# Performance work log

Measured on AMD Instinct MI355X. Metric: run time of the kernel, lower is better.

Reference implementation:

```python
import jax, jax.numpy as jnp
import numpy as np

B, S, E, H = 4, 2048, 1024, 16
D = E // H  # head dim = 64
NEG = -1e9


def setup_inputs() -> dict:
    key = jax.random.key(0)
    ks = jax.random.split(key, 6)
    scale = 1.0 / np.sqrt(E)
    return {
        "x": jax.random.normal(ks[0], (B, S, E), dtype=jnp.float32),
        "in_proj_weight": jax.random.normal(ks[1], (3 * E, E), dtype=jnp.float32) * scale,
        "in_proj_bias": jax.random.normal(ks[2], (3 * E,), dtype=jnp.float32) * 0.02,
        "out_proj_weight": jax.random.normal(ks[3], (E, E), dtype=jnp.float32) * scale,
        "out_proj_bias": jax.random.normal(ks[4], (E,), dtype=jnp.float32) * 0.02,
        "mask": jax.random.randint(ks[5], (B, S), 0, 2, dtype=jnp.int32),
    }


def reference(x, in_proj_weight, in_proj_bias, out_proj_weight, out_proj_bias, mask):
    # Equivalent of F.multi_head_attention_forward(h,h,h,...) with batch-first x.
    # qkv projection: [B,S,3E]
    qkv = jnp.einsum("bse,fe->bsf", x, in_proj_weight) + in_proj_bias
    q, k, v = jnp.split(qkv, 3, axis=-1)
    # split heads -> [B,S,H,D]
    q = q.reshape(B, S, H, D) * (1.0 / np.sqrt(D))
    k = k.reshape(B, S, H, D)
    v = v.reshape(B, S, H, D)
    # scores [B,H,Sq,Sk]
    scores = jnp.einsum("bqhd,bkhd->bhqk", q, k)
    # key_padding_mask = (mask == 0): True positions are excluded
    pad = (mask == 0)[:, None, None, :]  # [B,1,1,Sk]
    scores = jnp.where(pad, NEG, scores)
    attn = jax.nn.softmax(scores, axis=-1)
    # attention output -> [B,S,E]
    ctx = jnp.einsum("bhqk,bkhd->bqhd", attn, v).reshape(B, S, E)
    h_ = jnp.einsum("bse,fe->bsf", ctx, out_proj_weight) + out_proj_bias
    # residual; dropout is identity in eval mode
    return x + h_
```

## Files before the change

### kernel.cpp

```cpp
#include <hip/hip_runtime.h>
#include <stdint.h>
#include <math.h>

#define B_ 4
#define S_ 2048
#define E_ 1024
#define H_ 16
#define D_ 64
#define M_ (B_*S_)

typedef __attribute__((ext_vector_type(8))) short bf16x8;
typedef __attribute__((ext_vector_type(4))) float f32x4;

__device__ __forceinline__ unsigned short f2bf(float f) {
  union { float f; uint32_t u; } v; v.f = f;
  uint32_t u = v.u;
  return (unsigned short)((u + 0x7FFFu + ((u >> 16) & 1u)) >> 16);
}

__device__ __forceinline__ void gload16(const void* g, void* l) {
  __builtin_amdgcn_global_load_lds(
      (__attribute__((address_space(1))) void*)g,
      (__attribute__((address_space(3))) void*)l, 16, 0, 0);
}

__device__ __forceinline__ uint32_t cvtpk(float lo, float hi) {
  uint32_t r;
  asm("v_cvt_pk_bf16_f32 %0, %1, %2" : "=v"(r) : "v"(lo), "v"(hi));
  return r;
}

#define N1 ((M_*E_)/4)
#define N2 ((3*E_*E_)/4)
#define N3 ((E_*E_)/4)
#define NM ((B_*S_)/4)
__global__ __launch_bounds__(256) void cvt_all(const float* __restrict__ x,
                                               const float* __restrict__ w1,
                                               const float* __restrict__ w2,
                                               const int* __restrict__ mask,
                                               unsigned short* __restrict__ dst,
                                               float* __restrict__ maskf) {
  int i = blockIdx.x * 256 + threadIdx.x;
  if (i < N1 + N2 + N3) {
    const float* src;
    int j;
    if (i < N1) { src = x; j = i; }
    else if (i < N1 + N2) { src = w1; j = i - N1; }
    else { src = w2; j = i - N1 - N2; }
    float4 v = reinterpret_cast<const float4*>(src)[j];
    ushort4 o;
    o.x = f2bf(v.x); o.y = f2bf(v.y); o.z = f2bf(v.z); o.w = f2bf(v.w);
    reinterpret_cast<ushort4*>(dst)[i] = o;
  } else if (i < N1 + N2 + N3 + NM) {
    int j = i - (N1 + N2 + N3);
    int4 m = reinterpret_cast<const int4*>(mask)[j];
    float4 o;
    o.x = m.x ? 0.0f : -2.0e9f;
    o.y = m.y ? 0.0f : -2.0e9f;
    o.z = m.z ? 0.0f : -2.0e9f;
    o.w = m.w ? 0.0f : -2.0e9f;
    reinterpret_cast<float4*>(maskf)[j] = o;
  }
}

__global__ __launch_bounds__(256) void gemm_qkv128(
    const unsigned short* __restrict__ A,
    const unsigned short* __restrict__ W,
    const float* __restrict__ bias,
    unsigned short* __restrict__ Qg,
    unsigned short* __restrict__ Kg,
    unsigned short* __restrict__ Vtg)
{
  __shared__ __align__(16) unsigned short SMEM[17408];
  unsigned short* As = SMEM;
  unsigned short* Bs = SMEM + 8192;
  const int tid = threadIdx.x;
  const int lane = tid & 63;
  const int wave = tid >> 6;
  const int wm = (wave >> 1) * 64, wn = (wave & 1) * 64;
  const int l15 = lane & 15, lg = lane >> 4;

  const int orig = blockIdx.y * 24 + blockIdx.x;
  const int xcd = orig & 7;
  const int idx = orig >> 3;
  const int tn = (xcd * 3 + (idx % 3)) * 128;
  const int tm = (idx / 3) * 128;

  f32x4 zero4 = {0.f, 0.f, 0.f, 0.f};
  f32x4 acc[4][4];
  #pragma unroll
  for (int mi = 0; mi < 4; ++mi)
    #pragma unroll
    for (int ni = 0; ni < 4; ++ni) acc[mi][ni] = zero4;

  const int r0 = tid >> 3;
  const int cg = ((tid & 7) ^ (r0 & 7)) * 8;
  const unsigned short* Abase = A + (size_t)(tm + r0) * E_ + cg;
  const unsigned short* Bbase = W + (size_t)(tn + r0) * E_ + cg;
  unsigned short* lA = As + tid * 8;
  unsigned short* lB = Bs + tid * 8;

  int aoff[4], boff[4];
  #pragma unroll
  for (int i = 0; i < 4; ++i) {
    aoff[i] = (wm + i*16 + l15)*64 + ((lg ^ (l15 & 7)) * 8);
    boff[i] = (wn + i*16 + l15)*64 + ((lg ^ (l15 & 7)) * 8);
  }
  const int x4a = ((lg ^ 4 ^ (l15 & 7)) * 8) - ((lg ^ (l15 & 7)) * 8);

  for (int k0 = 0; k0 < E_; k0 += 64) {
    #pragma unroll
    for (int j = 0; j < 4; ++j)
      gload16(Abase + k0 + j*32*E_, lA + j*2048);
    #pragma unroll
    for (int j = 0; j < 4; ++j)
      gload16(Bbase + k0 + j*32*E_, lB + j*2048);
    __syncthreads();
    #pragma unroll
    for (int kc = 0; kc < 2; ++kc) {
      bf16x8 af[4], bfv[4];
      #pragma unroll
      for (int mi = 0; mi < 4; ++mi)
        af[mi] = *(const bf16x8*)&As[aoff[mi] + kc*x4a];
      #pragma unroll
      for (int ni = 0; ni < 4; ++ni)
        bfv[ni] = *(const bf16x8*)&Bs[boff[ni] + kc*x4a];
      #pragma unroll
      for (int mi = 0; mi < 4; ++mi)
        #pragma unroll
        for (int ni = 0; ni < 4; ++ni)
          acc[mi][ni] = __builtin_amdgcn_mfma_f32_16x16x32_bf16(af[mi], bfv[ni], acc[mi][ni], 0, 0, 0);
    }
    __syncthreads();
  }

  const int sec = tn >> 10;
  if (sec < 2) {
    #pragma unroll
    for (int ni = 0; ni < 4; ++ni) {
      const int col = tn + wn + ni*16 + l15;
      const float bcol = bias[col];
      const int f2 = col & 1023;
      const int h = f2 >> 6, d = f2 & 63;
      #pragma unroll
      for (int mi = 0; mi < 4; ++mi) {
        #pragma unroll
        for (int r = 0; r < 4; ++r) {
          const int row = tm + wm + mi*16 + lg*4 + r;
          const int b = row >> 11, s = row & (S_-1);
          const size_t bh = (size_t)(b * H_ + h);
          float val = acc[mi][ni][r] + bcol;
          if (sec == 0) {
            Qg[(bh*S_ + s)*D_ + d] = f2bf(val * 0.18033688f);
          } else {
            const int ch = (d >> 3) ^ (s & 7);
            Kg[(bh*S_ + s)*D_ + ch*8 + (d & 7)] = f2bf(val);
          }
        }
      }
    }
  } else {
    __syncthreads();
    unsigned short* T = SMEM;
    #pragma unroll
    for (int ni = 0; ni < 4; ++ni) {
      const int f = wn + ni*16 + l15;
      const float bcol = bias[tn + f];
      #pragma unroll
      for (int mi = 0; mi < 4; ++mi) {
        const int s0 = wm + mi*16 + lg*4;
        uint2 p;
        p.x = cvtpk(acc[mi][ni][0] + bcol, acc[mi][ni][1] + bcol);
        p.y = cvtpk(acc[mi][ni][2] + bcol, acc[mi][ni][3] + bcol);
        *reinterpret_cast<uint2*>(&T[f*136 + s0]) = p;
      }
    }
    __syncthreads();
    const int f = tid >> 1, sch = tid & 1;
    const int d = f & 63, hl = f >> 6;
    const int h = ((tn & 1023) >> 6) + hl;
    const int b = tm >> 11;
    const size_t bh = (size_t)(b * H_ + h);
    const int sbase = (tm & (S_-1)) + sch*64;
    unsigned short* vout = Vtg + (bh*D_ + d)*S_ + sbase;
    const unsigned short* tin = &T[f*136 + sch*64];
    #pragma unroll
    for (int j = 0; j < 8; ++j) {
      uint4 v = *reinterpret_cast<const uint4*>(&tin[j*8]);
      *reinterpret_cast<uint4*>(&vout[(j ^ (d & 7))*8]) = v;
    }
  }
}

__global__ __launch_bounds__(512, 4) void attn_fwd(
    const unsigned short* __restrict__ Qg,
    const unsigned short* __restrict__ Kg,
    const unsigned short* __restrict__ Vtg,
    const float* __restrict__ maskf,
    unsigned short* __restrict__ ctx)
{
  __shared__ __align__(16) unsigned char SMEM[36864];
  unsigned short* KsP = (unsigned short*)SMEM;
  unsigned short* VsP = (unsigned short*)(SMEM + 16384);
  const int tid = threadIdx.x, lane = tid & 63, wave = tid >> 6;
  const int l15 = lane & 15, lg = lane >> 4;

  const int lin = blockIdx.x;
  const int bh = (lin & 7) * 8 + (lin >> 6);
  const int qi = (lin >> 3) & 7;
  const int b = bh >> 4, h = bh & 15;
  const int q0 = qi * 256 + wave * 32;

  const unsigned short* Qb = Qg + (size_t)bh * S_ * D_;
  const unsigned short* Kb = Kg + (size_t)bh * S_ * D_;
  const unsigned short* Vb = Vtg + (size_t)bh * D_ * S_;
  const float* mrow = maskf + b * S_;

  bf16x8 qf[2][2];
  #pragma unroll
  for (int mi = 0; mi < 2; ++mi)
    #pragma unroll
    for (int kc = 0; kc < 2; ++kc)
      qf[mi][kc] = *(const bf16x8*)&Qb[(size_t)(q0 + mi*16 + l15)*D_ + kc*32 + lg*8];

  f32x4 zero4 = {0.f, 0.f, 0.f, 0.f};
  f32x4 accO[2][4];
  f32x4 accL[2] = {zero4, zero4};
  #pragma unroll
  for (int mi = 0; mi < 2; ++mi)
    #pragma unroll
    for (int df = 0; df < 4; ++df) accO[mi][df] = zero4;

  union { uint32_t u[4]; bf16x8 v; } ou;
  ou.u[0] = ou.u[1] = ou.u[2] = ou.u[3] = 0x3F803F80u;
  const bf16x8 onesv = ou.v;

  int kboff0[4], kboff1[4], vboff0[4], vboff1[4];
  #pragma unroll
  for (int kt = 0; kt < 4; ++kt) {
    const int krow = kt*16 + l15;
    kboff0[kt] = (krow*64 + ((lg ^ (krow & 7))*8)) * 2;
    kboff1[kt] = (krow*64 + (((4+lg) ^ (krow & 7))*8)) * 2;
  }
  #pragma unroll
  for (int df = 0; df < 4; ++df) {
    const int vrow = df*16 + l15;
    vboff0[df] = (vrow*64 + ((lg ^ (vrow & 7))*8)) * 2;
    vboff1[df] = (vrow*64 + (((4+lg) ^ (vrow & 7))*8)) * 2;
  }
  const char* KsB = (const char*)KsP;
  const char* VsB = (const char*)VsP;

  const int sr0 = tid >> 3, sc0 = (tid & 7) * 8;

  gload16(Kb + (size_t)sr0 * D_ + sc0, KsP + tid*8);
  gload16(Vb + (size_t)sr0 * S_ + sc0, VsP + tid*8);
  f32x4 mv0[4], mv1[4];
  #pragma unroll
  for (int kt = 0; kt < 4; ++kt)
    mv0[kt] = *(const f32x4*)&mrow[kt*16 + lg*4];
  const unsigned short* kpre = Kb + (size_t)(64 + sr0) * D_ + sc0;
  const unsigned short* vpre = Vb + (size_t)sr0 * S_ + 64 + sc0;
  const float* mpre = mrow + 64 + lg*4;
  __syncthreads();

#define ATTN_TILE(CUR, MVC, MVN, DO_PF)                                         \
  {                                                                             \
    if (DO_PF) {                                                                \
      gload16(kpre, KsP + ((CUR)^1)*4096 + tid*8);                              \
      gload16(vpre, VsP + ((CUR)^1)*4096 + tid*8);                              \
      kpre += 64*D_; vpre += 64;                                                \
      _Pragma("unroll")                                                         \
      for (int kt = 0; kt < 4; ++kt)                                            \
        MVN[kt] = *(const f32x4*)&mpre[kt*16];                                  \
      mpre += 64;                                                               \
    }                                                                           \
    f32x4 s_[2][4];                                                             \
    __builtin_amdgcn_s_setprio(1);                                              \
    _Pragma("unroll")                                                           \
    for (int kt = 0; kt < 4; ++kt) {                                            \
      bf16x8 kf0 = *(const bf16x8*)(KsB + (CUR)*8192 + kboff0[kt]);             \
      bf16x8 kf1 = *(const bf16x8*)(KsB + (CUR)*8192 + kboff1[kt]);             \
      s_[0][kt] = __builtin_amdgcn_mfma_f32_16x16x32_bf16(kf0, qf[0][0], MVC[kt], 0, 0, 0); \
      s_[0][kt] = __builtin_amdgcn_mfma_f32_16x16x32_bf16(kf1, qf[0][1], s_[0][kt], 0, 0, 0); \
      s_[1][kt] = __builtin_amdgcn_mfma_f32_16x16x32_bf16(kf0, qf[1][0], MVC[kt], 0, 0, 0); \
      s_[1][kt] = __builtin_amdgcn_mfma_f32_16x16x32_bf16(kf1, qf[1][1], s_[1][kt], 0, 0, 0); \
    }                                                                           \
    __builtin_amdgcn_s_setprio(0);                                              \
    _Pragma("unroll")                                                           \
    for (int mi = 0; mi < 2; ++mi)                                              \
      _Pragma("unroll")                                                         \
      for (int kt = 0; kt < 4; ++kt)                                            \
        _Pragma("unroll")                                                       \
        for (int r = 0; r < 4; ++r)                                             \
          s_[mi][kt][r] = __builtin_amdgcn_exp2f(s_[mi][kt][r]);                \
    bf16x8 pa[2][2];                                                            \
    _Pragma("unroll")                                                           \
    for (int mi = 0; mi < 2; ++mi) {                                            \
      _Pragma("unroll")                                                         \
      for (int kk = 0; kk < 2; ++kk) {                                          \
        uint32_t a0 = cvtpk(s_[mi][2*kk][0],   s_[mi][2*kk][1]);                \
        uint32_t c1 = cvtpk(s_[mi][2*kk][2],   s_[mi][2*kk][3]);                \
        uint32_t b0 = cvtpk(s_[mi][2*kk+1][0], s_[mi][2*kk+1][1]);              \
        uint32_t d1 = cvtpk(s_[mi][2*kk+1][2], s_[mi][2*kk+1][3]);              \
        asm("v_permlane32_swap_b32 %0, %1" : "+v"(a0), "+v"(b0));               \
        asm("v_permlane16_swap_b32 %0, %1" : "+v"(a0), "+v"(b0));               \
        asm("v_permlane32_swap_b32 %0, %1" : "+v"(c1), "+v"(d1));               \
        asm("v_permlane16_swap_b32 %0, %1" : "+v"(c1), "+v"(d1));               \
        union { bf16x8 v; uint32_t u[4]; } w;                                   \
        w.u[0] = a0; w.u[1] = c1; w.u[2] = b0; w.u[3] = d1;                     \
        pa[mi][kk] = w.v;                                                       \
      }                                                                         \
    }                                                                           \
    __builtin_amdgcn_s_setprio(1);                                              \
    accL[0] = __builtin_amdgcn_mfma_f32_16x16x32_bf16(pa[0][0], onesv, accL[0], 0, 0, 0); \
    accL[1] = __builtin_amdgcn_mfma_f32_16x16x32_bf16(pa[1][0], onesv, accL[1], 0, 0, 0); \
    _Pragma("unroll")                                                           \
    for (int df = 0; df < 4; ++df) {                                            \
      bf16x8 vf = *(const bf16x8*)(VsB + (CUR)*8192 + vboff0[df]);              \
      accO[0][df] = __builtin_amdgcn_mfma_f32_16x16x32_bf16(pa[0][0], vf, accO[0][df], 0, 0, 0); \
      accO[1][df] = __builtin_amdgcn_mfma_f32_16x16x32_bf16(pa[1][0], vf, accO[1][df], 0, 0, 0); \
    }                                                                           \
    accL[0] = __builtin_amdgcn_mfma_f32_16x16x32_bf16(pa[0][1], onesv, accL[0], 0, 0, 0); \
    accL[1] = __builtin_amdgcn_mfma_f32_16x16x32_bf16(pa[1][1], onesv, accL[1], 0, 0, 0); \
    _Pragma("unroll")                                                           \
    for (int df = 0; df < 4; ++df) {                                            \
      bf16x8 vf = *(const bf16x8*)(VsB + (CUR)*8192 + vboff1[df]);              \
      accO[0][df] = __builtin_amdgcn_mfma_f32_16x16x32_bf16(pa[0][1], vf, accO[0][df], 0, 0, 0); \
      accO[1][df] = __builtin_amdgcn_mfma_f32_16x16x32_bf16(pa[1][1], vf, accO[1][df], 0, 0, 0); \
    }                                                                           \
    __builtin_amdgcn_s_setprio(0);                                              \
    __syncthreads();                                                            \
  }

  for (int tt = 0; tt < 32; tt += 2) {
    ATTN_TILE(0, mv0, mv1, 1)
    ATTN_TILE(1, mv1, mv0, (tt < 30))
  }
#undef ATTN_TILE

  unsigned short* T = (unsigned short*)SMEM + wave * 2304;
  #pragma unroll
  for (int mi = 0; mi < 2; ++mi) {
    #pragma unroll
    for (int r = 0; r < 4; ++r) {
      const float iv = 1.0f / accL[mi][r];
      const int q = mi*16 + lg*4 + r;
      #pragma unroll
      for (int df = 0; df < 4; ++df)
        T[q*72 + df*16 + l15] = f2bf(accO[mi][df][r] * iv);
    }
  }
  __syncthreads();
  {
    const int g = lane >> 2, c4 = lane & 3;
    #pragma unroll
    for (int j2 = 0; j2 < 4; ++j2) {
      const int t = j2*16 + g;
      const int q = t >> 1, half = t & 1;
      uint4 v = *reinterpret_cast<const uint4*>(&T[q*72 + half*32 + c4*8]);
      const int srow = q0 + q;
      *reinterpret_cast<uint4*>(&ctx[((size_t)b*S_ + srow)*E_ + h*D_ + half*32 + c4*8]) = v;
    }
  }
}

__global__ __launch_bounds__(256) void gemm_out(
    const unsigned short* __restrict__ A,
    const unsigned short* __restrict__ W,
    const float* __restrict__ bias,
    const float* __restrict__ xres,
    float* __restrict__ out)
{
  __shared__ __align__(16) unsigned short As[128*64];
  __shared__ __align__(16) unsigned short Bs[128*64];
  const int tid = threadIdx.x;
  const int lane = tid & 63;
  const int wave = tid >> 6;
  const int wm = (wave >> 1) * 64, wn = (wave & 1) * 64;
  const int tm = blockIdx.y * 128, tn = blockIdx.x * 128;
  const int l15 = lane & 15, lg = lane >> 4;

  f32x4 zero4 = {0.f, 0.f, 0.f, 0.f};
  f32x4 acc[4][4];
  #pragma unroll
  for (int mi = 0; mi < 4; ++mi)
    #pragma unroll
    for (int ni = 0; ni < 4; ++ni) acc[mi][ni] = zero4;

  const int r0 = tid >> 3;
  const int cg = ((tid & 7) ^ (r0 & 7)) * 8;
  const unsigned short* Abase = A + (size_t)(tm + r0) * E_ + cg;
  const unsigned short* Bbase = W + (size_t)(tn + r0) * E_ + cg;
  unsigned short* lA = As + tid * 8;
  unsigned short* lB = Bs + tid * 8;

  int aoff[4], boff[4];
  #pragma unroll
  for (int i = 0; i < 4; ++i) {
    aoff[i] = (wm + i*16 + l15)*64 + ((lg ^ (l15 & 7)) * 8);
    boff[i] = (wn + i*16 + l15)*64 + ((lg ^ (l15 & 7)) * 8);
  }
  const int x4a = ((lg ^ 4 ^ (l15 & 7)) * 8) - ((lg ^ (l15 & 7)) * 8);

  for (int k0 = 0; k0 < E_; k0 += 64) {
    #pragma unroll
    for (int j = 0; j < 4; ++j)
      gload16(Abase + k0 + j*32*E_, lA + j*2048);
    #pragma unroll
    for (int j = 0; j < 4; ++j)
      gload16(Bbase + k0 + j*32*E_, lB + j*2048);
    __syncthreads();
    #pragma unroll
    for (int kc = 0; kc < 2; ++kc) {
      bf16x8 af[4], bfv[4];
      #pragma unroll
      for (int mi = 0; mi < 4; ++mi)
        af[mi] = *(const bf16x8*)&As[aoff[mi] + kc*x4a];
      #pragma unroll
      for (int ni = 0; ni < 4; ++ni)
        bfv[ni] = *(const bf16x8*)&Bs[boff[ni] + kc*x4a];
      #pragma unroll
      for (int mi = 0; mi < 4; ++mi)
        #pragma unroll
        for (int ni = 0; ni < 4; ++ni)
          acc[mi][ni] = __builtin_amdgcn_mfma_f32_16x16x32_bf16(af[mi], bfv[ni], acc[mi][ni], 0, 0, 0);
    }
    __syncthreads();
  }

  #pragma unroll
  for (int ni = 0; ni < 4; ++ni) {
    const int col = tn + wn + ni*16 + l15;
    const float bcol = bias[col];
    #pragma unroll
    for (int mi = 0; mi < 4; ++mi) {
      #pragma unroll
      for (int r = 0; r < 4; ++r) {
        const int row = tm + wm + mi*16 + lg*4 + r;
        out[(size_t)row*E_ + col] = xres[(size_t)row*E_ + col] + acc[mi][ni][r] + bcol;
      }
    }
  }
}

extern "C" void kernel_launch(void* const* d_in, const int* in_sizes, int n_in,
                              void* d_out, int out_size, void* d_ws, size_t ws_size,
                              hipStream_t stream) {
  const float* x  = (const float*)d_in[0];
  const float* w1 = (const float*)d_in[1];
  const float* b1 = (const float*)d_in[2];
  const float* w2 = (const float*)d_in[3];
  const float* b2 = (const float*)d_in[4];
  const int* mask = (const int*)d_in[5];
  float* out = (float*)d_out;

  const size_t SZ = (size_t)B_*H_*S_*D_;
  unsigned short* Qg  = (unsigned short*)d_ws;
  unsigned short* Kg  = Qg + SZ;
  unsigned short* Vtg = Kg + SZ;
  unsigned short* xb  = Vtg + SZ;
  unsigned short* w1b = xb + (size_t)M_*E_;
  unsigned short* w2b = w1b + (size_t)3*E_*E_;
  float* maskf = (float*)(w2b + (size_t)E_*E_);
  unsigned short* ctx = xb;

  const int ntot = N1 + N2 + N3 + NM;
  cvt_all<<<(ntot + 255)/256, 256, 0, stream>>>(x, w1, w2, mask, xb, maskf);

  gemm_qkv128<<<dim3(24, 64), 256, 0, stream>>>(xb, w1b, b1, Qg, Kg, Vtg);
  attn_fwd<<<512, 512, 0, stream>>>(Qg, Kg, Vtg, maskf, ctx);
  gemm_out<<<dim3(E_/128, M_/128), 256, 0, stream>>>(ctx, w2b, b2, x, out);
}
```

Before: 199.6 us.

## Give each attention wave 64 query rows with 256-thread blocks

The attention kernel now runs 4 waves per block instead of 8, and each wave handles 64 query rows instead of 32. Each K/V fragment read from LDS therefore feeds four MFMAs instead of two, cutting LDS traffic per unit of math. Score computation is split into two halves to limit live registers, and the mask bias is loaded per tile instead of being prefetched. The costs are higher register pressure and fewer waves per block, which may reduce occupancy and latency hiding.

```diff
diff --git a/kernel.cpp b/kernel.cpp
--- a/kernel.cpp
+++ b/kernel.cpp
@@ -192,7 +192,7 @@
   }
 }
 
-__global__ __launch_bounds__(512, 4) void attn_fwd(
+__global__ __launch_bounds__(256) void attn_fwd(
     const unsigned short* __restrict__ Qg,
     const unsigned short* __restrict__ Kg,
     const unsigned short* __restrict__ Vtg,
@@ -209,25 +209,25 @@
   const int bh = (lin & 7) * 8 + (lin >> 6);
   const int qi = (lin >> 3) & 7;
   const int b = bh >> 4, h = bh & 15;
-  const int q0 = qi * 256 + wave * 32;
+  const int q0 = qi * 256 + wave * 64;
 
   const unsigned short* Qb = Qg + (size_t)bh * S_ * D_;
   const unsigned short* Kb = Kg + (size_t)bh * S_ * D_;
   const unsigned short* Vb = Vtg + (size_t)bh * D_ * S_;
   const float* mrow = maskf + b * S_;
 
-  bf16x8 qf[2][2];
-  #pragma unroll
-  for (int mi = 0; mi < 2; ++mi)
+  bf16x8 qf[4][2];
+  #pragma unroll
+  for (int mi = 0; mi < 4; ++mi)
     #pragma unroll
     for (int kc = 0; kc < 2; ++kc)
       qf[mi][kc] = *(const bf16x8*)&Qb[(size_t)(q0 + mi*16 + l15)*D_ + kc*32 + lg*8];
 
   f32x4 zero4 = {0.f, 0.f, 0.f, 0.f};
-  f32x4 accO[2][4];
-  f32x4 accL[2] = {zero4, zero4};
-  #pragma unroll
-  for (int mi = 0; mi < 2; ++mi)
+  f32x4 accO[4][4];
+  f32x4 accL[4] = {zero4, zero4, zero4, zero4};
+  #pragma unroll
+  for (int mi = 0; mi < 4; ++mi)
     #pragma unroll
     for (int df = 0; df < 4; ++df) accO[mi][df] = zero4;
 
@@ -235,18 +235,16 @@
   ou.u[0] = ou.u[1] = ou.u[2] = ou.u[3] = 0x3F803F80u;
   const bf16x8 onesv = ou.v;
 
-  int kboff0[4], kboff1[4], vboff0[4], vboff1[4];
+  int kboff[4], vboff[4];
   #pragma unroll
   for (int kt = 0; kt < 4; ++kt) {
     const int krow = kt*16 + l15;
-    kboff0[kt] = (krow*64 + ((lg ^ (krow & 7))*8)) * 2;
-    kboff1[kt] = (krow*64 + (((4+lg) ^ (krow & 7))*8)) * 2;
+    kboff[kt] = (krow*64 + ((lg ^ (krow & 7))*8)) * 2;
   }
   #pragma unroll
   for (int df = 0; df < 4; ++df) {
     const int vrow = df*16 + l15;
-    vboff0[df] = (vrow*64 + ((lg ^ (vrow & 7))*8)) * 2;
-    vboff1[df] = (vrow*64 + (((4+lg) ^ (vrow & 7))*8)) * 2;
+    vboff[df] = (vrow*64 + ((lg ^ (vrow & 7))*8)) * 2;
   }
   const char* KsB = (const char*)KsP;
   const char* VsB = (const char*)VsP;
@@ -254,94 +252,95 @@
   const int sr0 = tid >> 3, sc0 = (tid & 7) * 8;
 
   gload16(Kb + (size_t)sr0 * D_ + sc0, KsP + tid*8);
+  gload16(Kb + (size_t)(sr0 + 32) * D_ + sc0, KsP + (tid+256)*8);
   gload16(Vb + (size_t)sr0 * S_ + sc0, VsP + tid*8);
-  f32x4 mv0[4], mv1[4];
-  #pragma unroll
-  for (int kt = 0; kt < 4; ++kt)
-    mv0[kt] = *(const f32x4*)&mrow[kt*16 + lg*4];
+  gload16(Vb + (size_t)(sr0 + 32) * S_ + sc0, VsP + (tid+256)*8);
   const unsigned short* kpre = Kb + (size_t)(64 + sr0) * D_ + sc0;
   const unsigned short* vpre = Vb + (size_t)sr0 * S_ + 64 + sc0;
-  const float* mpre = mrow + 64 + lg*4;
+  const float* mcur = mrow + lg*4;
   __syncthreads();
 
-#define ATTN_TILE(CUR, MVC, MVN, DO_PF)                                         \
+#define ATTN_TILE(CUR, DO_PF)                                                   \
   {                                                                             \
     if (DO_PF) {                                                                \
       gload16(kpre, KsP + ((CUR)^1)*4096 + tid*8);                              \
+      gload16(kpre + 32*D_, KsP + ((CUR)^1)*4096 + (tid+256)*8);                \
       gload16(vpre, VsP + ((CUR)^1)*4096 + tid*8);                              \
+      gload16(vpre + 32*S_, VsP + ((CUR)^1)*4096 + (tid+256)*8);                \
       kpre += 64*D_; vpre += 64;                                                \
+    }                                                                           \
+                                        \
+    f32x4 mv[4];                                                                \
+    _Pragma("unroll")                                                           \
+    for (int kt = 0; kt < 4; ++kt)                                              \
+      mv[kt] = *(const f32x4*)&mcur[kt*16];                                     \
+    mcur += 64;                                                                 \
+    bf16x8 pa[4][2];                                                            \
+    _Pragma("unroll")                                                           \
+    for (int kth = 0; kth < 2; ++kth) {                                         \
+      f32x4 s_[4][2];                                                           \
+      __builtin_amdgcn_s_setprio(1);                                            \
       _Pragma("unroll")                                                         \
-      for (int kt = 0; kt < 4; ++kt)                                            \
-        MVN[kt] = *(const f32x4*)&mpre[kt*16];                                  \
-      mpre += 64;                                                               \
-    }                                                                           \
-    f32x4 s_[2][4];                                                             \
-    __builtin_amdgcn_s_setprio(1);                                              \
-    _Pragma("unroll")                                                           \
-    for (int kt = 0; kt < 4; ++kt) {                                            \
-      bf16x8 kf0 = *(const bf16x8*)(KsB + (CUR)*8192 + kboff0[kt]);             \
-      bf16x8 kf1 = *(const bf16x8*)(KsB + (CUR)*8192 + kboff1[kt]);             \
-      s_[0][kt] = __builtin_amdgcn_mfma_f32_16x16x32_bf16(kf0, qf[0][0], MVC[kt], 0, 0, 0); \
-      s_[0][kt] = __builtin_amdgcn_mfma_f32_16x16x32_bf16(kf1, qf[0][1], s_[0][kt], 0, 0, 0); \
-      s_[1][kt] = __builtin_amdgcn_mfma_f32_16x16x32_bf16(kf0, qf[1][0], MVC[kt], 0, 0, 0); \
-      s_[1][kt] = __builtin_amdgcn_mfma_f32_16x16x32_bf16(kf1, qf[1][1], s_[1][kt], 0, 0, 0); \
-    }                                                                           \
-    __builtin_amdgcn_s_setprio(0);                                              \
-    _Pragma("unroll")                                                           \
-    for (int mi = 0; mi < 2; ++mi)                                              \
+      for (int k2 = 0; k2 < 2; ++k2) {                                          \
+        const int kt = kth*2 + k2;                                              \
+        bf16x8 kf0 = *(const bf16x8*)(KsB + (CUR)*8192 + kboff[kt]);            \
+        bf16x8 kf1 = *(const bf16x8*)(KsB + (CUR)*8192 + (kboff[kt] ^ 64));     \
+        _Pragma("unroll")                                                       \
+        for (int mi = 0; mi < 4; ++mi) {                                        \
+          s_[mi][k2] = __builtin_amdgcn_mfma_f32_16x16x32_bf16(kf0, qf[mi][0], mv[kt], 0, 0, 0); \
+          s_[mi][k2] = __builtin_amdgcn_mfma_f32_16x16x32_bf16(kf1, qf[mi][1], s_[mi][k2], 0, 0, 0); \
+        }                                                                       \
+      }                                                                         \
+      __builtin_amdgcn_s_setprio(0);                                            \
       _Pragma("unroll")                                                         \
-      for (int kt = 0; kt < 4; ++kt)                                            \
+      for (int mi = 0; mi < 4; ++mi)                                            \
         _Pragma("unroll")                                                       \
-        for (int r = 0; r < 4; ++r)                                             \
-          s_[mi][kt][r] = __builtin_amdgcn_exp2f(s_[mi][kt][r]);                \
-    bf16x8 pa[2][2];                                                            \
-    _Pragma("unroll")                                                           \
-    for (int mi = 0; mi < 2; ++mi) {                                            \
+        for (int k2 = 0; k2 < 2; ++k2)                                          \
+          _Pragma("unroll")                                                     \
+          for (int r = 0; r < 4; ++r)                                           \
+            s_[mi][k2][r] = __builtin_amdgcn_exp2f(s_[mi][k2][r]);              \
       _Pragma("unroll")                                                         \
-      for (int kk = 0; kk < 2; ++kk) {                                          \
-        uint32_t a0 = cvtpk(s_[mi][2*kk][0],   s_[mi][2*kk][1]);                \
-        uint32_t c1 = cvtpk(s_[mi][2*kk][2],   s_[mi][2*kk][3]);                \
-        uint32_t b0 = cvtpk(s_[mi][2*kk+1][0], s_[mi][2*kk+1][1]);              \
-        uint32_t d1 = cvtpk(s_[mi][2*kk+1][2], s_[mi][2*kk+1][3]);              \
+      for (int mi = 0; mi < 4; ++mi) {                                          \
+        uint32_t a0 = cvtpk(s_[mi][0][0], s_[mi][0][1]);                        \
+        uint32_t c1 = cvtpk(s_[mi][0][2], s_[mi][0][3]);                        \
+        uint32_t b0 = cvtpk(s_[mi][1][0], s_[mi][1][1]);                        \
+        uint32_t d1 = cvtpk(s_[mi][1][2], s_[mi][1][3]);                        \
         asm("v_permlane32_swap_b32 %0, %1" : "+v"(a0), "+v"(b0));               \
         asm("v_permlane16_swap_b32 %0, %1" : "+v"(a0), "+v"(b0));               \
         asm("v_permlane32_swap_b32 %0, %1" : "+v"(c1), "+v"(d1));               \
         asm("v_permlane16_swap_b32 %0, %1" : "+v"(c1), "+v"(d1));               \
         union { bf16x8 v; uint32_t u[4]; } w;                                   \
         w.u[0] = a0; w.u[1] = c1; w.u[2] = b0; w.u[3] = d1;                     \
-        pa[mi][kk] = w.v;                                                       \
+        pa[mi][kth] = w.v;                                                      \
       }                                                                         \
     }                                                                           \
     __builtin_amdgcn_s_setprio(1);                                              \
-    accL[0] = __builtin_amdgcn_mfma_f32_16x16x32_bf16(pa[0][0], onesv, accL[0], 0, 0, 0); \
-    accL[1] = __builtin_amdgcn_mfma_f32_16x16x32_bf16(pa[1][0], onesv, accL[1], 0, 0, 0); \
     _Pragma("unroll")                                                           \
-    for (int df = 0; df < 4; ++df) {                                            \
-      bf16x8 vf = *(const bf16x8*)(VsB + (CUR)*8192 + vboff0[df]);              \
-      accO[0][df] = __builtin_amdgcn_mfma_f32_16x16x32_bf16(pa[0][0], vf, accO[0][df], 0, 0, 0); \
-      accO[1][df] = __builtin_amdgcn_mfma_f32_16x16x32_bf16(pa[1][0], vf, accO[1][df], 0, 0, 0); \
-    }                                                                           \
-    accL[0] = __builtin_amdgcn_mfma_f32_16x16x32_bf16(pa[0][1], onesv, accL[0], 0, 0, 0); \
-    accL[1] = __builtin_amdgcn_mfma_f32_16x16x32_bf16(pa[1][1], onesv, accL[1], 0, 0, 0); \
-    _Pragma("unroll")                                                           \
-    for (int df = 0; df < 4; ++df) {                                            \
-      bf16x8 vf = *(const bf16x8*)(VsB + (CUR)*8192 + vboff1[df]);              \
-      accO[0][df] = __builtin_amdgcn_mfma_f32_16x16x32_bf16(pa[0][1], vf, accO[0][df], 0, 0, 0); \
-      accO[1][df] = __builtin_amdgcn_mfma_f32_16x16x32_bf16(pa[1][1], vf, accO[1][df], 0, 0, 0); \
+    for (int kk = 0; kk < 2; ++kk) {                                            \
+      _Pragma("unroll")                                                         \
+      for (int mi = 0; mi < 4; ++mi)                                            \
+        accL[mi] = __builtin_amdgcn_mfma_f32_16x16x32_bf16(pa[mi][kk], onesv, accL[mi], 0, 0, 0); \
+      _Pragma("unroll")                                                         \
+      for (int df = 0; df < 4; ++df) {                                          \
+        bf16x8 vf = *(const bf16x8*)(VsB + (CUR)*8192 + (vboff[df] ^ (kk*64))); \
+        _Pragma("unroll")                                                       \
+        for (int mi = 0; mi < 4; ++mi)                                          \
+          accO[mi][df] = __builtin_amdgcn_mfma_f32_16x16x32_bf16(pa[mi][kk], vf, accO[mi][df], 0, 0, 0); \
+      }                                                                         \
     }                                                                           \
     __builtin_amdgcn_s_setprio(0);                                              \
     __syncthreads();                                                            \
   }
 
   for (int tt = 0; tt < 32; tt += 2) {
-    ATTN_TILE(0, mv0, mv1, 1)
-    ATTN_TILE(1, mv1, mv0, (tt < 30))
+    ATTN_TILE(0, 1)
+    ATTN_TILE(1, (tt < 30))
   }
 #undef ATTN_TILE
 
-  unsigned short* T = (unsigned short*)SMEM + wave * 2304;
-  #pragma unroll
-  for (int mi = 0; mi < 2; ++mi) {
+  unsigned short* T = (unsigned short*)SMEM + wave * 4608;
+  #pragma unroll
+  for (int mi = 0; mi < 4; ++mi) {
     #pragma unroll
     for (int r = 0; r < 4; ++r) {
       const float iv = 1.0f / accL[mi][r];
@@ -355,7 +354,7 @@
   {
     const int g = lane >> 2, c4 = lane & 3;
     #pragma unroll
-    for (int j2 = 0; j2 < 4; ++j2) {
+    for (int j2 = 0; j2 < 8; ++j2) {
       const int t = j2*16 + g;
       const int q = t >> 1, half = t & 1;
       uint4 v = *reinterpret_cast<const uint4*>(&T[q*72 + half*32 + c4*8]);
@@ -469,6 +468,6 @@
   cvt_all<<<(ntot + 255)/256, 256, 0, stream>>>(x, w1, w2, mask, xb, maskf);
 
   gemm_qkv128<<<dim3(24, 64), 256, 0, stream>>>(xb, w1b, b1, Qg, Kg, Vtg);
-  attn_fwd<<<512, 512, 0, stream>>>(Qg, Kg, Vtg, maskf, ctx);
+  attn_fwd<<<512, 256, 0, stream>>>(Qg, Kg, Vtg, maskf, ctx);
   gemm_out<<<dim3(E_/128, M_/128), 256, 0, stream>>>(ctx, w2b, b2, x, out);
 }
```

After: 232.0 us. 16.3% more time.

## Stage 128-key epochs in attention to halve block barriers

Applied to the files above, without the earlier changes.

The attention kernel now loads K/V tiles in 128-key epochs, two 64-key subtiles per buffer, with double buffering, and synchronises once per epoch instead of once per 64 keys. Mask values are now loaded inside each subtile instead of being prefetched one tile ahead. This removes half of the __syncthreads barriers and issues larger prefetches. In exchange, LDS use grows from 36 KB to 64 KB per block, which may lower occupancy below the requested 4 blocks per CU, and mask-load latency is now exposed.

```diff
diff --git a/kernel.cpp b/kernel.cpp
--- a/kernel.cpp
+++ b/kernel.cpp
@@ -199,9 +199,9 @@
     const float* __restrict__ maskf,
     unsigned short* __restrict__ ctx)
 {
-  __shared__ __align__(16) unsigned char SMEM[36864];
+  __shared__ __align__(16) unsigned char SMEM[65536];
   unsigned short* KsP = (unsigned short*)SMEM;
-  unsigned short* VsP = (unsigned short*)(SMEM + 16384);
+  unsigned short* VsP = (unsigned short*)(SMEM + 32768);
   const int tid = threadIdx.x, lane = tid & 63, wave = tid >> 6;
   const int l15 = lane & 15, lg = lane >> 4;
 
@@ -253,37 +253,30 @@
 
   const int sr0 = tid >> 3, sc0 = (tid & 7) * 8;
 
-  gload16(Kb + (size_t)sr0 * D_ + sc0, KsP + tid*8);
-  gload16(Vb + (size_t)sr0 * S_ + sc0, VsP + tid*8);
-  f32x4 mv0[4], mv1[4];
-  #pragma unroll
-  for (int kt = 0; kt < 4; ++kt)
-    mv0[kt] = *(const f32x4*)&mrow[kt*16 + lg*4];
-  const unsigned short* kpre = Kb + (size_t)(64 + sr0) * D_ + sc0;
-  const unsigned short* vpre = Vb + (size_t)sr0 * S_ + 64 + sc0;
-  const float* mpre = mrow + 64 + lg*4;
+  gload16(Kb + (size_t)sr0 * D_ + sc0,        KsP + tid*8);
+  gload16(Kb + (size_t)(sr0 + 64) * D_ + sc0, KsP + (tid+512)*8);
+  gload16(Vb + (size_t)sr0 * S_ + sc0,        VsP + tid*8);
+  gload16(Vb + (size_t)sr0 * S_ + 64 + sc0,   VsP + (tid+512)*8);
+  const unsigned short* kpre = Kb + (size_t)(128 + sr0) * D_ + sc0;
+  const unsigned short* vpre = Vb + (size_t)sr0 * S_ + 128 + sc0;
+  const float* mcur = mrow + lg*4;
   __syncthreads();
 
-#define ATTN_TILE(CUR, MVC, MVN, DO_PF)                                         \
+#define SUBTILE(KT, VT, MOFF)                                                   \
   {                                                                             \
-    if (DO_PF) {                                                                \
-      gload16(kpre, KsP + ((CUR)^1)*4096 + tid*8);                              \
-      gload16(vpre, VsP + ((CUR)^1)*4096 + tid*8);                              \
-      kpre += 64*D_; vpre += 64;                                                \
-      _Pragma("unroll")                                                         \
-      for (int kt = 0; kt < 4; ++kt)                                            \
-        MVN[kt] = *(const f32x4*)&mpre[kt*16];                                  \
-      mpre += 64;                                                               \
-    }                                                                           \
+    f32x4 mv[4];                                                                \
+    _Pragma("unroll")                                                           \
+    for (int kt = 0; kt < 4; ++kt)                                              \
+      mv[kt] = *(const f32x4*)&mcur[(MOFF) + kt*16];                            \
     f32x4 s_[2][4];                                                             \
     __builtin_amdgcn_s_setprio(1);                                              \
     _Pragma("unroll")                                                           \
     for (int kt = 0; kt < 4; ++kt) {                                            \
-      bf16x8 kf0 = *(const bf16x8*)(KsB + (CUR)*8192 + kboff0[kt]);             \
-      bf16x8 kf1 = *(const bf16x8*)(KsB + (CUR)*8192 + kboff1[kt]);             \
-      s_[0][kt] = __builtin_amdgcn_mfma_f32_16x16x32_bf16(kf0, qf[0][0], MVC[kt], 0, 0, 0); \
+      bf16x8 kf0 = *(const bf16x8*)((KT) + kboff0[kt]);                         \
+      bf16x8 kf1 = *(const bf16x8*)((KT) + kboff1[kt]);                         \
+      s_[0][kt] = __builtin_amdgcn_mfma_f32_16x16x32_bf16(kf0, qf[0][0], mv[kt], 0, 0, 0); \
       s_[0][kt] = __builtin_amdgcn_mfma_f32_16x16x32_bf16(kf1, qf[0][1], s_[0][kt], 0, 0, 0); \
-      s_[1][kt] = __builtin_amdgcn_mfma_f32_16x16x32_bf16(kf0, qf[1][0], MVC[kt], 0, 0, 0); \
+      s_[1][kt] = __builtin_amdgcn_mfma_f32_16x16x32_bf16(kf0, qf[1][0], mv[kt], 0, 0, 0); \
       s_[1][kt] = __builtin_amdgcn_mfma_f32_16x16x32_bf16(kf1, qf[1][1], s_[1][kt], 0, 0, 0); \
     }                                                                           \
     __builtin_amdgcn_s_setprio(0);                                              \
@@ -317,7 +310,7 @@
     accL[1] = __builtin_amdgcn_mfma_f32_16x16x32_bf16(pa[1][0], onesv, accL[1], 0, 0, 0); \
     _Pragma("unroll")                                                           \
     for (int df = 0; df < 4; ++df) {                                            \
-      bf16x8 vf = *(const bf16x8*)(VsB + (CUR)*8192 + vboff0[df]);              \
+      bf16x8 vf = *(const bf16x8*)((VT) + vboff0[df]);                          \
       accO[0][df] = __builtin_amdgcn_mfma_f32_16x16x32_bf16(pa[0][0], vf, accO[0][df], 0, 0, 0); \
       accO[1][df] = __builtin_amdgcn_mfma_f32_16x16x32_bf16(pa[1][0], vf, accO[1][df], 0, 0, 0); \
     }                                                                           \
@@ -325,19 +318,34 @@
     accL[1] = __builtin_amdgcn_mfma_f32_16x16x32_bf16(pa[1][1], onesv, accL[1], 0, 0, 0); \
     _Pragma("unroll")                                                           \
     for (int df = 0; df < 4; ++df) {                                            \
-      bf16x8 vf = *(const bf16x8*)(VsB + (CUR)*8192 + vboff1[df]);              \
+      bf16x8 vf = *(const bf16x8*)((VT) + vboff1[df]);                          \
       accO[0][df] = __builtin_amdgcn_mfma_f32_16x16x32_bf16(pa[0][1], vf, accO[0][df], 0, 0, 0); \
       accO[1][df] = __builtin_amdgcn_mfma_f32_16x16x32_bf16(pa[1][1], vf, accO[1][df], 0, 0, 0); \
     }                                                                           \
     __builtin_amdgcn_s_setprio(0);                                              \
+  }
+
+#define EPOCH(CUR, DO_PF)                                                       \
+  {                                                                             \
+    if (DO_PF) {                                                                \
+      gload16(kpre,           KsP + ((CUR)^1)*8192 + tid*8);                    \
+      gload16(kpre + 64*D_,   KsP + ((CUR)^1)*8192 + (tid+512)*8);              \
+      gload16(vpre,           VsP + ((CUR)^1)*8192 + tid*8);                    \
+      gload16(vpre + 64,      VsP + ((CUR)^1)*8192 + (tid+512)*8);              \
+      kpre += 128*D_; vpre += 128;                                              \
+    }                                                                           \
+    SUBTILE(KsB + (CUR)*16384,        VsB + (CUR)*16384,        0)              \
+    SUBTILE(KsB + (CUR)*16384 + 8192, VsB + (CUR)*16384 + 8192, 64)             \
+    mcur += 128;                                                                \
     __syncthreads();                                                            \
   }
 
-  for (int tt = 0; tt < 32; tt += 2) {
-    ATTN_TILE(0, mv0, mv1, 1)
-    ATTN_TILE(1, mv1, mv0, (tt < 30))
-  }
-#undef ATTN_TILE
+  for (int ee = 0; ee < 16; ee += 2) {
+    EPOCH(0, 1)
+    EPOCH(1, (ee < 14))
+  }
+#undef EPOCH
+#undef SUBTILE
 
   unsigned short* T = (unsigned short*)SMEM + wave * 2304;
   #pragma unroll
```

Result: faster. 190.1 us (-4.8%).
